# Kernel tuning notes

Hardware: AMD Instinct MI355X
Metric: run time of the kernel (lower is better)

## Reference

```python
import jax, jax.numpy as jnp
import numpy as np

ALPHA = 1.0          # gating temperature (train_alpha=False)
DEPTH = 4            # floor(log2(leaves=16))
LEAF_NUM = 16        # 2**DEPTH
N_INTERNAL = LEAF_NUM - 2  # nodes 1..14 (root handled separately)
B, D, OUT = 8192, 512, 64


def _prob(x, pw, aW, ab):
    # vectorized Node.prob with set_comps=True (comparators recomputed from batch mean)
    comp = -jnp.mean(x * pw, axis=0)                      # [in]
    dist = jax.nn.sigmoid(ALPHA * (pw * x + comp))        # [B, in]
    attn = jax.nn.softmax(x @ aW.T + ab, axis=-1)         # [B, in]
    return jnp.sum(dist * attn, axis=1, keepdims=True)    # [B, 1]


def setup_inputs() -> dict:
    key = jax.random.key(0)
    ks = jax.random.split(key, 12)
    s = 0.02
    return {
        "x": jax.random.normal(ks[0], (B, D), jnp.float32),
        # root node (input_size=D, output_size=D)
        "calc_W0": jax.random.normal(ks[1], (D, D), jnp.float32) * s,
        "calc_b0": jnp.zeros((D,), jnp.float32),
        "prob_w0": jax.random.uniform(ks[2], (D,), jnp.float32),
        "attn_W0": jax.random.normal(ks[3], (D, D), jnp.float32) * s,
        "attn_b0": jnp.zeros((D,), jnp.float32),
        # internal nodes 1..14 (input_size=2D, output_size=D), stacked
        "calc_W": jax.random.normal(ks[4], (N_INTERNAL, D, 2 * D), jnp.float32) * s,
        "calc_b": jnp.zeros((N_INTERNAL, D), jnp.float32),
        "prob_w": jax.random.uniform(ks[5], (N_INTERNAL, 2 * D), jnp.float32),
        "attn_W": jax.random.normal(ks[6], (N_INTERNAL, 2 * D, 2 * D), jnp.float32) * s,
        "attn_b": jnp.zeros((N_INTERNAL, 2 * D), jnp.float32),
        # leaf nodes: learned output vectors (torch.rand init)
        "leaf_out": jax.random.uniform(ks[7], (LEAF_NUM, OUT), jnp.float32),
    }


def reference(x, calc_W0, calc_b0, prob_w0, attn_W0, attn_b0,
              calc_W, calc_b, prob_w, attn_W, attn_b, leaf_out):
    outs, probab = {}, {}
    # root
    outs[0] = jax.nn.relu(x @ calc_W0.T + calc_b0)            # [B, D]
    p = _prob(x, prob_w0, attn_W0, attn_b0)                   # [B, 1]
    probab[1] = 1.0 - p
    probab[2] = p
    # internal nodes 1..leaf_num-2 (binary-tree routing)
    for n in range(1, LEAF_NUM - 1):
        parent = (n - 1) // 2
        inp = jnp.concatenate([outs[parent], x], axis=1)      # [B, 2D]
        outs[n] = jax.nn.relu(inp @ calc_W[n - 1].T + calc_b[n - 1])
        p = _prob(inp, prob_w[n - 1], attn_W[n - 1], attn_b[n - 1])
        probab[2 * n + 1] = probab[n] * (1.0 - p)
        probab[2 * n + 2] = probab[n] * p
    # leaves: indices LEAF_NUM-1 .. 2*LEAF_NUM-2
    leaf_p = jnp.concatenate([probab[i + LEAF_NUM - 1] for i in range(LEAF_NUM)], axis=1)  # [B, 16]
    # sum over leaves of probab * leaf_out == leaf_p @ leaf_out
    actions = leaf_p @ leaf_out                                # [B, OUT]
    return jax.nn.softmax(actions, axis=-1)
```

## Files before the change

kernel.cpp:

```cpp
#include <hip/hip_runtime.h>
#include <hip/hip_bf16.h>
#include <cstdint>


#define NROWS 8192
#define HALFD 512

typedef __bf16 bf16x8 __attribute__((ext_vector_type(8)));
typedef short  short8 __attribute__((ext_vector_type(8)));
typedef float  f32x4  __attribute__((ext_vector_type(4)));

union FragU { short8 s; bf16x8 b; };

struct GArgs {
  const __hip_bfloat16* A0[4];
  const __hip_bfloat16* Bw[4];
  const float* bias[4];
  const float* pw[4];
  const float* cm0[4];
  __hip_bfloat16* outB[4];
  float* S1[4];
  float* S2[4];
};

__device__ __forceinline__ void gl2lds16(const void* g, void* l) {
  __builtin_amdgcn_global_load_lds((__attribute__((address_space(1))) void*)g,
                                   (__attribute__((address_space(3))) void*)l,
                                   16, 0, 0);
}

__global__ void k_f32_to_bf16(const float* __restrict__ s,
                              __hip_bfloat16* __restrict__ d, int n) {
  int i = (blockIdx.x * 256 + threadIdx.x) * 4;
  if (i >= n) return;
  float4 v = *(const float4*)(s + i);
  union { short4 s4; __hip_bfloat16 h[4]; } u;
  u.h[0] = __float2bfloat16(v.x);
  u.h[1] = __float2bfloat16(v.y);
  u.h[2] = __float2bfloat16(v.z);
  u.h[3] = __float2bfloat16(v.w);
  *(short4*)(d + i) = u.s4;
}

__global__ void k_colsum_f32(const float* __restrict__ src, float* __restrict__ dst) {
  int c  = blockIdx.x * 256 + threadIdx.x;
  int r0 = blockIdx.y * 256;
  float s = 0.f;
  for (int r = 0; r < 256; ++r) s += src[(size_t)(r0 + r) * HALFD + c];
  atomicAdd(&dst[c], s);
}
__global__ void k_colsum_bf16(const __hip_bfloat16* __restrict__ src0,
                              float* __restrict__ dst0) {
  const __hip_bfloat16* src = src0 + (size_t)blockIdx.z * NROWS * HALFD;
  float* dst = dst0 + (size_t)blockIdx.z * 512;
  int c  = blockIdx.x * 256 + threadIdx.x;
  int r0 = blockIdx.y * 256;
  float s = 0.f;
  for (int r = 0; r < 256; ++r) s += __bfloat162float(src[(size_t)(r0 + r) * HALFD + c]);
  atomicAdd(&dst[c], s);
}

template <int MODE>
__global__ __launch_bounds__(256, 2)
void k_gemm(GArgs ga, const __hip_bfloat16* __restrict__ A1,
            const float* __restrict__ cm1, int K) {
  __shared__ alignas(16) short As[128 * 64];
  __shared__ alignas(16) short Bs[128 * 64];

  const int z = blockIdx.z;
  const __hip_bfloat16* __restrict__ Ah0 = ga.A0[z];
  const __hip_bfloat16* __restrict__ Bw  = ga.Bw[z];
  const float* __restrict__ bias = ga.bias[z];

  const int tid  = threadIdx.x;
  const int lane = tid & 63;
  const int wv   = tid >> 6;
  const int wm   = wv >> 1, wn = wv & 1;
  const int lr   = lane & 15, lg = lane >> 4;
  const int row0 = blockIdx.y * 128;
  const int col0 = blockIdx.x * 128;

  f32x4 acc[4][4];
#pragma unroll
  for (int i = 0; i < 4; ++i)
#pragma unroll
    for (int j = 0; j < 4; ++j)
#pragma unroll
      for (int e = 0; e < 4; ++e) acc[i][j][e] = 0.f;

  const int sr = tid >> 3;
  const int sc = (((tid & 7) ^ (sr & 7)) << 3);
  const int sw = lr & 7;

  for (int kt = 0; kt < K; kt += 64) {
    const __hip_bfloat16* Asrc = (kt < HALFD) ? Ah0 : A1;
    const int kl = kt & (HALFD - 1);
    __syncthreads();
#pragma unroll
    for (int rnd = 0; rnd < 4; ++rnd) {
      const int r = rnd * 32 + sr;
      gl2lds16(Asrc + (size_t)(row0 + r) * HALFD + kl + sc,
               (char*)As + rnd * 4096 + wv * 1024);
      gl2lds16(Bw + (size_t)(col0 + r) * K + kt + sc,
               (char*)Bs + rnd * 4096 + wv * 1024);
    }
    __syncthreads();
#pragma unroll
    for (int kk = 0; kk < 64; kk += 32) {
      FragU a[4], b[4];
#pragma unroll
      for (int mi = 0; mi < 4; ++mi)
        a[mi].s = *(const short8*)(As + (wm * 64 + mi * 16 + lr) * 64 +
                                   ((((kk >> 3) + lg) ^ sw) << 3));
#pragma unroll
      for (int ni = 0; ni < 4; ++ni)
        b[ni].s = *(const short8*)(Bs + (wn * 64 + ni * 16 + lr) * 64 +
                                   ((((kk >> 3) + lg) ^ sw) << 3));
#pragma unroll
      for (int mi = 0; mi < 4; ++mi)
#pragma unroll
        for (int ni = 0; ni < 4; ++ni)
          acc[mi][ni] = __builtin_amdgcn_mfma_f32_16x16x32_bf16(a[mi].b, b[ni].b,
                                                               acc[mi][ni], 0, 0, 0);
    }
  }

  if constexpr (MODE == 0) {
    __hip_bfloat16* outB = ga.outB[z];
#pragma unroll
    for (int ni = 0; ni < 4; ++ni) {
      const int col  = col0 + wn * 64 + ni * 16 + lr;
      const float bv = bias[col];
      __hip_bfloat16* op = outB + (size_t)(col >> 9) * ((size_t)NROWS * HALFD) + (col & 511);
#pragma unroll
      for (int mi = 0; mi < 4; ++mi) {
#pragma unroll
        for (int rg = 0; rg < 4; ++rg) {
          const int row = row0 + wm * 64 + mi * 16 + lg * 4 + rg;
          float v = acc[mi][ni][rg] + bv;
          v = v > 0.f ? v : 0.f;
          op[(size_t)row * HALFD] = __float2bfloat16(v);
        }
      }
    }
  } else {
    const float* __restrict__ pw  = ga.pw[z];
    const float* __restrict__ cm0 = ga.cm0[z];
    const int node = col0 >> 10;
    float* s1p = ga.S1[z] + (size_t)node * NROWS;
    float* s2p = ga.S2[z] + (size_t)node * NROWS;
    float bv[4], pwv[4], cmv[4];
    const __hip_bfloat16* Ain[4];
#pragma unroll
    for (int ni = 0; ni < 4; ++ni) {
      const int col = col0 + wn * 64 + ni * 16 + lr;
      bv[ni]  = bias[col];
      pwv[ni] = pw[col];
      const int ii   = col & 1023;
      const int half = ii >> 9;
      const int cc   = ii & 511;
      cmv[ni] = (half ? cm1[cc] : cm0[cc]) * (1.f / 8192.f);
      Ain[ni] = (half ? A1 : Ah0) + cc;
    }
#pragma unroll
    for (int mi = 0; mi < 4; ++mi) {
#pragma unroll
      for (int rg = 0; rg < 4; ++rg) {
        const int row = row0 + wm * 64 + mi * 16 + lg * 4 + rg;
        float s1 = 0.f, s2 = 0.f;
#pragma unroll
        for (int ni = 0; ni < 4; ++ni) {
          const float l = acc[mi][ni][rg] + bv[ni];
          const float e = __expf(l);
          const float inpv = __bfloat162float(Ain[ni][(size_t)row * HALFD]);
          const float zz = pwv[ni] * (inpv - cmv[ni]);
          const float dist = 1.f / (1.f + __expf(-zz));
          s1 += e;
          s2 += dist * e;
        }
#pragma unroll
        for (int off = 1; off < 16; off <<= 1) {
          s1 += __shfl_xor(s1, off);
          s2 += __shfl_xor(s2, off);
        }
        if (lr == 0) {
          atomicAdd(&s1p[row], s1);
          atomicAdd(&s2p[row], s2);
        }
      }
    }
  }
}

__global__ void k_finalize(const float* __restrict__ S1, const float* __restrict__ S2,
                           const float* __restrict__ leaf_out, float* __restrict__ out) {
  const int r    = (blockIdx.x * 256 + threadIdx.x) >> 6;
  const int lane = threadIdx.x & 63;
  float pb[31];
  pb[0] = 1.f;
#pragma unroll
  for (int n = 0; n < 15; ++n) {
    const float p = S2[(size_t)n * NROWS + r] / S1[(size_t)n * NROWS + r];
    pb[2 * n + 1] = pb[n] * (1.f - p);
    pb[2 * n + 2] = pb[n] * p;
  }
  float a = 0.f;
#pragma unroll
  for (int i = 0; i < 16; ++i) a += pb[15 + i] * leaf_out[i * 64 + lane];
  float m = a;
#pragma unroll
  for (int off = 1; off < 64; off <<= 1) m = fmaxf(m, __shfl_xor(m, off));
  const float e = __expf(a - m);
  float s = e;
#pragma unroll
  for (int off = 1; off < 64; off <<= 1) s += __shfl_xor(s, off);
  out[(size_t)r * 64 + lane] = e / s;
}

static constexpr size_t O_S1   = 0;
static constexpr size_t O_S2   = O_S1 + (size_t)15 * NROWS * 4;
static constexpr size_t O_XSUM = O_S2 + (size_t)15 * NROWS * 4;
static constexpr size_t O_CS   = O_XSUM + 512 * 4;
static constexpr size_t O_ZEND = O_CS + 7 * 512 * 4;
static constexpr size_t O_XB   = O_ZEND;
static constexpr size_t O_OUTS = O_XB + (size_t)NROWS * HALFD * 2;
static constexpr size_t O_CW0  = O_OUTS + 7 * (size_t)NROWS * HALFD * 2;
static constexpr size_t O_AW0  = O_CW0 + (size_t)512 * 512 * 2;
static constexpr size_t O_CW   = O_AW0 + (size_t)512 * 512 * 2;
static constexpr size_t O_AW   = O_CW + (size_t)14 * 512 * 1024 * 2;

extern "C" void kernel_launch(void* const* d_in, const int* in_sizes, int n_in,
                              void* d_out, int out_size, void* d_ws, size_t ws_size,
                              hipStream_t stream) {
  const float* x        = (const float*)d_in[0];
  const float* calc_b0  = (const float*)d_in[2];
  const float* prob_w0  = (const float*)d_in[3];
  const float* attn_b0  = (const float*)d_in[5];
  const float* calc_b   = (const float*)d_in[7];
  const float* prob_w   = (const float*)d_in[8];
  const float* attn_b   = (const float*)d_in[10];
  const float* leaf_out = (const float*)d_in[11];
  float* out = (float*)d_out;
  char* ws = (char*)d_ws;

  float* S1   = (float*)(ws + O_S1);
  float* S2   = (float*)(ws + O_S2);
  float* xsum = (float*)(ws + O_XSUM);
  float* cs   = (float*)(ws + O_CS);
  __hip_bfloat16* xb   = (__hip_bfloat16*)(ws + O_XB);
  __hip_bfloat16* outs = (__hip_bfloat16*)(ws + O_OUTS);
  __hip_bfloat16* cW0b = (__hip_bfloat16*)(ws + O_CW0);
  __hip_bfloat16* aW0b = (__hip_bfloat16*)(ws + O_AW0);
  __hip_bfloat16* cWb  = (__hip_bfloat16*)(ws + O_CW);
  __hip_bfloat16* aWb  = (__hip_bfloat16*)(ws + O_AW);
  const size_t OSZ = (size_t)NROWS * HALFD;

  hipMemsetAsync(d_ws, 0, O_ZEND, stream);

  auto cvt = [&](const float* s, __hip_bfloat16* d, int n) {
    k_f32_to_bf16<<<dim3((n / 4 + 255) / 256), 256, 0, stream>>>(s, d, n);
  };
  cvt(x, xb, NROWS * HALFD);
  cvt((const float*)d_in[1], cW0b, 512 * 512);
  cvt((const float*)d_in[4], aW0b, 512 * 512);
  cvt((const float*)d_in[6], cWb, 14 * 512 * 1024);
  cvt((const float*)d_in[9], aWb, 14 * 1024 * 1024);
  k_colsum_f32<<<dim3(2, 32), 256, 0, stream>>>(x, xsum);

  auto calcG = [&](int nz, int N, const __hip_bfloat16* const* A0,
                   const __hip_bfloat16* const* Bw, const float* const* bp,
                   __hip_bfloat16* const* ob) {
    GArgs ga{};
    for (int i = 0; i < nz; ++i) {
      ga.A0[i] = A0[i]; ga.Bw[i] = Bw[i]; ga.bias[i] = bp[i]; ga.outB[i] = ob[i];
    }
    k_gemm<0><<<dim3(N / 128, 64, nz), 256, 0, stream>>>(ga, xb, xsum, N == 512 ? 512 : 1024);
  };
  auto attnG = [&](int nz, int N, const __hip_bfloat16* const* A0,
                   const __hip_bfloat16* const* Bw, const float* const* bp,
                   const float* const* pwp, const float* const* c0,
                   const int* nodeBase) {
    GArgs ga{};
    for (int i = 0; i < nz; ++i) {
      ga.A0[i] = A0[i]; ga.Bw[i] = Bw[i]; ga.bias[i] = bp[i];
      ga.pw[i] = pwp[i]; ga.cm0[i] = c0[i];
      ga.S1[i] = S1 + (size_t)nodeBase[i] * NROWS;
      ga.S2[i] = S2 + (size_t)nodeBase[i] * NROWS;
    }
    k_gemm<1><<<dim3(N / 128, 64, nz), 256, 0, stream>>>(ga, xb, xsum, N == 512 ? 512 : 1024);
  };
  auto colsum = [&](int first, int cnt) {
    k_colsum_bf16<<<dim3(2, 32, cnt), 256, 0, stream>>>(outs + (size_t)first * OSZ,
                                                        cs + (size_t)first * 512);
  };

  { const __hip_bfloat16* A0[1] = {xb};  const __hip_bfloat16* Bw[1] = {cW0b};
    const float* bp[1] = {calc_b0};      __hip_bfloat16* ob[1] = {outs};
    calcG(1, 512, A0, Bw, bp, ob); }
  { const __hip_bfloat16* A0[1] = {xb};  const __hip_bfloat16* Bw[1] = {aW0b};
    const float* bp[1] = {attn_b0};      const float* pwp[1] = {prob_w0};
    const float* c0[1] = {xsum};         int nb[1] = {0};
    attnG(1, 512, A0, Bw, bp, pwp, c0, nb); }
  colsum(0, 1);

  { const __hip_bfloat16* A0[1] = {outs};  const __hip_bfloat16* Bw[1] = {cWb};
    const float* bp[1] = {calc_b};         __hip_bfloat16* ob[1] = {outs + OSZ};
    calcG(1, 1024, A0, Bw, bp, ob); }
  { const __hip_bfloat16* A0[1] = {outs};  const __hip_bfloat16* Bw[1] = {aWb};
    const float* bp[1] = {attn_b};         const float* pwp[1] = {prob_w};
    const float* c0[1] = {cs};             int nb[1] = {1};
    attnG(1, 2048, A0, Bw, bp, pwp, c0, nb); }
  colsum(1, 2);

  { const __hip_bfloat16* A0[2] = {outs + OSZ, outs + 2 * OSZ};
    const __hip_bfloat16* Bw[2] = {cWb + (size_t)2 * 512 * 1024, cWb + (size_t)4 * 512 * 1024};
    const float* bp[2] = {calc_b + 2 * 512, calc_b + 4 * 512};
    __hip_bfloat16* ob[2] = {outs + 3 * OSZ, outs + 5 * OSZ};
    calcG(2, 1024, A0, Bw, bp, ob); }
  { const __hip_bfloat16* A0[2] = {outs + OSZ, outs + 2 * OSZ};
    const __hip_bfloat16* Bw[2] = {aWb + (size_t)2 * 1024 * 1024, aWb + (size_t)4 * 1024 * 1024};
    const float* bp[2] = {attn_b + 2 * 1024, attn_b + 4 * 1024};
    const float* pwp[2] = {prob_w + 2 * 1024, prob_w + 4 * 1024};
    const float* c0[2] = {cs + 512, cs + 2 * 512};
    int nb[2] = {3, 5};
    attnG(2, 2048, A0, Bw, bp, pwp, c0, nb); }
  colsum(3, 4);

  { const __hip_bfloat16* A0[4] = {outs + 3 * OSZ, outs + 4 * OSZ, outs + 5 * OSZ, outs + 6 * OSZ};
    const __hip_bfloat16* Bw[4] = {aWb + (size_t)6 * 1024 * 1024, aWb + (size_t)8 * 1024 * 1024,
                                   aWb + (size_t)10 * 1024 * 1024, aWb + (size_t)12 * 1024 * 1024};
    const float* bp[4] = {attn_b + 6 * 1024, attn_b + 8 * 1024,
                          attn_b + 10 * 1024, attn_b + 12 * 1024};
    const float* pwp[4] = {prob_w + 6 * 1024, prob_w + 8 * 1024,
                           prob_w + 10 * 1024, prob_w + 12 * 1024};
    const float* c0[4] = {cs + 3 * 512, cs + 4 * 512, cs + 5 * 512, cs + 6 * 512};
    int nb[4] = {7, 9, 11, 13};
    attnG(4, 2048, A0, Bw, bp, pwp, c0, nb); }

  k_finalize<<<NROWS * 64 / 256, 256, 0, stream>>>(S1, S2, leaf_out, out);
}
```

Before: 615.0 us.

## Merge calc and attn GEMMs per level, fuse column sums, batch conversions

Calc and attention GEMMs of the same tree level now share one launch, with the mode selected at runtime per z-slice. Grids are padded and extra x-blocks exit early. Column sums of the relu outputs are accumulated in the GEMM epilogue via shuffles and atomics, replacing separate colsum kernels. The five f32->bf16 conversions become one launch, and blocks are remapped so rows are grouped by XCD for L2 locality. This cuts launch count and an extra pass over the outputs, at the cost of a runtime mode branch, idle padding blocks and atomic contention.

Result: faster. 535.2 us (-13.0%).

```diff
diff --git a/kernel.cpp b/kernel.cpp
--- a/kernel.cpp
+++ b/kernel.cpp
@@ -19,8 +19,12 @@
   const float* pw[4];
   const float* cm0[4];
   __hip_bfloat16* outB[4];
+  float* csOut[4];
   float* S1[4];
   float* S2[4];
+  int mode[4];
+  int gx[4];
+  int K[4];
 };
 
 __device__ __forceinline__ void gl2lds16(const void* g, void* l) {
@@ -29,17 +33,18 @@
                                    16, 0, 0);
 }
 
-__global__ void k_f32_to_bf16(const float* __restrict__ s,
-                              __hip_bfloat16* __restrict__ d, int n) {
-  int i = (blockIdx.x * 256 + threadIdx.x) * 4;
-  if (i >= n) return;
-  float4 v = *(const float4*)(s + i);
+struct CvtArgs { const float* src[5]; __hip_bfloat16* dst[5]; int nblk[5]; };
+__global__ void k_cvt(CvtArgs a) {
+  int b = blockIdx.x, r = 0;
+  while (b >= a.nblk[r]) { b -= a.nblk[r]; ++r; }
+  const int i = (b * 256 + threadIdx.x) * 4;
+  float4 v = *(const float4*)(a.src[r] + i);
   union { short4 s4; __hip_bfloat16 h[4]; } u;
   u.h[0] = __float2bfloat16(v.x);
   u.h[1] = __float2bfloat16(v.y);
   u.h[2] = __float2bfloat16(v.z);
   u.h[3] = __float2bfloat16(v.w);
-  *(short4*)(d + i) = u.s4;
+  *(short4*)(a.dst[r] + i) = u.s4;
 }
 
 __global__ void k_colsum_f32(const float* __restrict__ src, float* __restrict__ dst) {
@@ -49,36 +54,33 @@
   for (int r = 0; r < 256; ++r) s += src[(size_t)(r0 + r) * HALFD + c];
   atomicAdd(&dst[c], s);
 }
-__global__ void k_colsum_bf16(const __hip_bfloat16* __restrict__ src0,
-                              float* __restrict__ dst0) {
-  const __hip_bfloat16* src = src0 + (size_t)blockIdx.z * NROWS * HALFD;
-  float* dst = dst0 + (size_t)blockIdx.z * 512;
-  int c  = blockIdx.x * 256 + threadIdx.x;
-  int r0 = blockIdx.y * 256;
-  float s = 0.f;
-  for (int r = 0; r < 256; ++r) s += __bfloat162float(src[(size_t)(r0 + r) * HALFD + c]);
-  atomicAdd(&dst[c], s);
-}
-
-template <int MODE>
+
 __global__ __launch_bounds__(256, 2)
 void k_gemm(GArgs ga, const __hip_bfloat16* __restrict__ A1,
-            const float* __restrict__ cm1, int K) {
+            const float* __restrict__ cm1) {
   __shared__ alignas(16) short As[128 * 64];
   __shared__ alignas(16) short Bs[128 * 64];
 
   const int z = blockIdx.z;
+  const int id  = blockIdx.x + gridDim.x * blockIdx.y;
+  const int xcd = id & 7;
+  const int q   = id >> 3;
+  const int bx  = q >> 3;
+  const int by  = xcd * 8 + (q & 7);
+  if (bx >= ga.gx[z]) return;
+
   const __hip_bfloat16* __restrict__ Ah0 = ga.A0[z];
   const __hip_bfloat16* __restrict__ Bw  = ga.Bw[z];
   const float* __restrict__ bias = ga.bias[z];
+  const int K = ga.K[z];
 
   const int tid  = threadIdx.x;
   const int lane = tid & 63;
   const int wv   = tid >> 6;
   const int wm   = wv >> 1, wn = wv & 1;
   const int lr   = lane & 15, lg = lane >> 4;
-  const int row0 = blockIdx.y * 128;
-  const int col0 = blockIdx.x * 128;
+  const int row0 = by * 128;
+  const int col0 = bx * 128;
 
   f32x4 acc[4][4];
 #pragma unroll
@@ -125,13 +127,15 @@
     }
   }
 
-  if constexpr (MODE == 0) {
+  if (ga.mode[z] == 0) {
     __hip_bfloat16* outB = ga.outB[z];
+    float* csOut = ga.csOut[z];
 #pragma unroll
     for (int ni = 0; ni < 4; ++ni) {
       const int col  = col0 + wn * 64 + ni * 16 + lr;
       const float bv = bias[col];
       __hip_bfloat16* op = outB + (size_t)(col >> 9) * ((size_t)NROWS * HALFD) + (col & 511);
+      float csum = 0.f;
 #pragma unroll
       for (int mi = 0; mi < 4; ++mi) {
 #pragma unroll
@@ -139,9 +143,13 @@
           const int row = row0 + wm * 64 + mi * 16 + lg * 4 + rg;
           float v = acc[mi][ni][rg] + bv;
           v = v > 0.f ? v : 0.f;
+          csum += v;
           op[(size_t)row * HALFD] = __float2bfloat16(v);
         }
       }
+      csum += __shfl_xor(csum, 16);
+      csum += __shfl_xor(csum, 32);
+      if (lg == 0) atomicAdd(&csOut[col], csum);
     }
   } else {
     const float* __restrict__ pw  = ga.pw[z];
@@ -257,85 +265,77 @@
 
   hipMemsetAsync(d_ws, 0, O_ZEND, stream);
 
-  auto cvt = [&](const float* s, __hip_bfloat16* d, int n) {
-    k_f32_to_bf16<<<dim3((n / 4 + 255) / 256), 256, 0, stream>>>(s, d, n);
-  };
-  cvt(x, xb, NROWS * HALFD);
-  cvt((const float*)d_in[1], cW0b, 512 * 512);
-  cvt((const float*)d_in[4], aW0b, 512 * 512);
-  cvt((const float*)d_in[6], cWb, 14 * 512 * 1024);
-  cvt((const float*)d_in[9], aWb, 14 * 1024 * 1024);
+  {
+    CvtArgs ca{};
+    ca.src[0] = x;                     ca.dst[0] = xb;   ca.nblk[0] = NROWS * HALFD / 1024;
+    ca.src[1] = (const float*)d_in[1]; ca.dst[1] = cW0b; ca.nblk[1] = 512 * 512 / 1024;
+    ca.src[2] = (const float*)d_in[4]; ca.dst[2] = aW0b; ca.nblk[2] = 512 * 512 / 1024;
+    ca.src[3] = (const float*)d_in[6]; ca.dst[3] = cWb;  ca.nblk[3] = 14 * 512 * 1024 / 1024;
+    ca.src[4] = (const float*)d_in[9]; ca.dst[4] = aWb;  ca.nblk[4] = 14 * 1024 * 1024 / 1024;
+    int tot = ca.nblk[0] + ca.nblk[1] + ca.nblk[2] + ca.nblk[3] + ca.nblk[4];
+    k_cvt<<<tot, 256, 0, stream>>>(ca);
+  }
   k_colsum_f32<<<dim3(2, 32), 256, 0, stream>>>(x, xsum);
 
-  auto calcG = [&](int nz, int N, const __hip_bfloat16* const* A0,
-                   const __hip_bfloat16* const* Bw, const float* const* bp,
-                   __hip_bfloat16* const* ob) {
+  {
     GArgs ga{};
-    for (int i = 0; i < nz; ++i) {
-      ga.A0[i] = A0[i]; ga.Bw[i] = Bw[i]; ga.bias[i] = bp[i]; ga.outB[i] = ob[i];
-    }
-    k_gemm<0><<<dim3(N / 128, 64, nz), 256, 0, stream>>>(ga, xb, xsum, N == 512 ? 512 : 1024);
-  };
-  auto attnG = [&](int nz, int N, const __hip_bfloat16* const* A0,
-                   const __hip_bfloat16* const* Bw, const float* const* bp,
-                   const float* const* pwp, const float* const* c0,
-                   const int* nodeBase) {
+    ga.mode[0] = 0; ga.gx[0] = 4; ga.K[0] = 512;
+    ga.A0[0] = xb; ga.Bw[0] = cW0b; ga.bias[0] = calc_b0;
+    ga.outB[0] = outs; ga.csOut[0] = cs;
+    ga.mode[1] = 1; ga.gx[1] = 4; ga.K[1] = 512;
+    ga.A0[1] = xb; ga.Bw[1] = aW0b; ga.bias[1] = attn_b0;
+    ga.pw[1] = prob_w0; ga.cm0[1] = xsum;
+    ga.S1[1] = S1; ga.S2[1] = S2;
+    k_gemm<<<dim3(4, 64, 2), 256, 0, stream>>>(ga, xb, xsum);
+  }
+  {
     GArgs ga{};
-    for (int i = 0; i < nz; ++i) {
-      ga.A0[i] = A0[i]; ga.Bw[i] = Bw[i]; ga.bias[i] = bp[i];
-      ga.pw[i] = pwp[i]; ga.cm0[i] = c0[i];
-      ga.S1[i] = S1 + (size_t)nodeBase[i] * NROWS;
-      ga.S2[i] = S2 + (size_t)nodeBase[i] * NROWS;
-    }
-    k_gemm<1><<<dim3(N / 128, 64, nz), 256, 0, stream>>>(ga, xb, xsum, N == 512 ? 512 : 1024);
-  };
-  auto colsum = [&](int first, int cnt) {
-    k_colsum_bf16<<<dim3(2, 32, cnt), 256, 0, stream>>>(outs + (size_t)first * OSZ,
-                                                        cs + (size_t)first * 512);
-  };
-
-  { const __hip_bfloat16* A0[1] = {xb};  const __hip_bfloat16* Bw[1] = {cW0b};
-    const float* bp[1] = {calc_b0};      __hip_bfloat16* ob[1] = {outs};
-    calcG(1, 512, A0, Bw, bp, ob); }
-  { const __hip_bfloat16* A0[1] = {xb};  const __hip_bfloat16* Bw[1] = {aW0b};
-    const float* bp[1] = {attn_b0};      const float* pwp[1] = {prob_w0};
-    const float* c0[1] = {xsum};         int nb[1] = {0};
-    attnG(1, 512, A0, Bw, bp, pwp, c0, nb); }
-  colsum(0, 1);
-
-  { const __hip_bfloat16* A0[1] = {outs};  const __hip_bfloat16* Bw[1] = {cWb};
-    const float* bp[1] = {calc_b};         __hip_bfloat16* ob[1] = {outs + OSZ};
-    calcG(1, 1024, A0, Bw, bp, ob); }
-  { const __hip_bfloat16* A0[1] = {outs};  const __hip_bfloat16* Bw[1] = {aWb};
-    const float* bp[1] = {attn_b};         const float* pwp[1] = {prob_w};
-    const float* c0[1] = {cs};             int nb[1] = {1};
-    attnG(1, 2048, A0, Bw, bp, pwp, c0, nb); }
-  colsum(1, 2);
-
-  { const __hip_bfloat16* A0[2] = {outs + OSZ, outs + 2 * OSZ};
-    const __hip_bfloat16* Bw[2] = {cWb + (size_t)2 * 512 * 1024, cWb + (size_t)4 * 512 * 1024};
-    const float* bp[2] = {calc_b + 2 * 512, calc_b + 4 * 512};
-    __hip_bfloat16* ob[2] = {outs + 3 * OSZ, outs + 5 * OSZ};
-    calcG(2, 1024, A0, Bw, bp, ob); }
-  { const __hip_bfloat16* A0[2] = {outs + OSZ, outs + 2 * OSZ};
-    const __hip_bfloat16* Bw[2] = {aWb + (size_t)2 * 1024 * 1024, aWb + (size_t)4 * 1024 * 1024};
-    const float* bp[2] = {attn_b + 2 * 1024, attn_b + 4 * 1024};
-    const float* pwp[2] = {prob_w + 2 * 1024, prob_w + 4 * 1024};
-    const float* c0[2] = {cs + 512, cs + 2 * 512};
-    int nb[2] = {3, 5};
-    attnG(2, 2048, A0, Bw, bp, pwp, c0, nb); }
-  colsum(3, 4);
-
-  { const __hip_bfloat16* A0[4] = {outs + 3 * OSZ, outs + 4 * OSZ, outs + 5 * OSZ, outs + 6 * OSZ};
-    const __hip_bfloat16* Bw[4] = {aWb + (size_t)6 * 1024 * 1024, aWb + (size_t)8 * 1024 * 1024,
-                                   aWb + (size_t)10 * 1024 * 1024, aWb + (size_t)12 * 1024 * 1024};
-    const float* bp[4] = {attn_b + 6 * 1024, attn_b + 8 * 1024,
-                          attn_b + 10 * 1024, attn_b + 12 * 1024};
-    const float* pwp[4] = {prob_w + 6 * 1024, prob_w + 8 * 1024,
-                           prob_w + 10 * 1024, prob_w + 12 * 1024};
-    const float* c0[4] = {cs + 3 * 512, cs + 4 * 512, cs + 5 * 512, cs + 6 * 512};
-    int nb[4] = {7, 9, 11, 13};
-    attnG(4, 2048, A0, Bw, bp, pwp, c0, nb); }
+    ga.mode[0] = 0; ga.gx[0] = 8; ga.K[0] = 1024;
+    ga.A0[0] = outs; ga.Bw[0] = cWb; ga.bias[0] = calc_b;
+    ga.outB[0] = outs + OSZ; ga.csOut[0] = cs + 512;
+    ga.mode[1] = 1; ga.gx[1] = 16; ga.K[1] = 1024;
+    ga.A0[1] = outs; ga.Bw[1] = aWb; ga.bias[1] = attn_b;
+    ga.pw[1] = prob_w; ga.cm0[1] = cs;
+    ga.S1[1] = S1 + (size_t)1 * NROWS; ga.S2[1] = S2 + (size_t)1 * NROWS;
+    k_gemm<<<dim3(16, 64, 2), 256, 0, stream>>>(ga, xb, xsum);
+  }
+  {
+    GArgs ga{};
+    for (int i = 0; i < 2; ++i) {
+      ga.mode[i] = 0; ga.gx[i] = 8; ga.K[i] = 1024;
+      ga.A0[i] = outs + (size_t)(1 + i) * OSZ;
+      ga.Bw[i] = cWb + (size_t)(2 + 2 * i) * 512 * 1024;
+      ga.bias[i] = calc_b + (2 + 2 * i) * 512;
+      ga.outB[i] = outs + (size_t)(3 + 2 * i) * OSZ;
+      ga.csOut[i] = cs + (size_t)(3 + 2 * i) * 512;
+    }
+    for (int i = 0; i < 2; ++i) {
+      const int zi = 2 + i;
+      ga.mode[zi] = 1; ga.gx[zi] = 16; ga.K[zi] = 1024;
+      ga.A0[zi] = outs + (size_t)(1 + i) * OSZ;
+      ga.Bw[zi] = aWb + (size_t)(2 + 2 * i) * 1024 * 1024;
+      ga.bias[zi] = attn_b + (2 + 2 * i) * 1024;
+      ga.pw[zi] = prob_w + (2 + 2 * i) * 1024;
+      ga.cm0[zi] = cs + (size_t)(1 + i) * 512;
+      ga.S1[zi] = S1 + (size_t)(3 + 2 * i) * NROWS;
+      ga.S2[zi] = S2 + (size_t)(3 + 2 * i) * NROWS;
+    }
+    k_gemm<<<dim3(16, 64, 4), 256, 0, stream>>>(ga, xb, xsum);
+  }
+  {
+    GArgs ga{};
+    for (int i = 0; i < 4; ++i) {
+      ga.mode[i] = 1; ga.gx[i] = 16; ga.K[i] = 1024;
+      ga.A0[i] = outs + (size_t)(3 + i) * OSZ;
+      ga.Bw[i] = aWb + (size_t)(6 + 2 * i) * 1024 * 1024;
+      ga.bias[i] = attn_b + (6 + 2 * i) * 1024;
+      ga.pw[i] = prob_w + (6 + 2 * i) * 1024;
+      ga.cm0[i] = cs + (size_t)(3 + i) * 512;
+      ga.S1[i] = S1 + (size_t)(7 + 2 * i) * NROWS;
+      ga.S2[i] = S2 + (size_t)(7 + 2 * i) * NROWS;
+    }
+    k_gemm<<<dim3(16, 64, 4), 256, 0, stream>>>(ga, xb, xsum);
+  }
 
   k_finalize<<<NROWS * 64 / 256, 256, 0, stream>>>(S1, S2, leaf_out, out);
 }
```
